# Kernel optimization log

Measured on AMD Instinct MI355X. Metric: run time of the kernel, lower is better.

## Reference

```python
import jax, jax.numpy as jnp
import numpy as np

D_MODEL = 1024
D_FF = 4096


def _layernorm(x, g, b, eps=1e-5):
    mu = jnp.mean(x, axis=-1, keepdims=True)
    var = jnp.var(x, axis=-1, keepdims=True)
    return (x - mu) * jax.lax.rsqrt(var + eps) * g + b


def setup_inputs() -> dict:
    key = jax.random.key(0)
    ks = jax.random.split(key, 16)
    d, f = D_MODEL, D_FF
    s = 1.0 / np.sqrt(d)
    inp = {
        'x': jax.random.normal(ks[0], (4, 2048, d), dtype=jnp.float32),
        'wq': jax.random.uniform(ks[1], (d, d), jnp.float32, -s, s),
        'bq': jax.random.uniform(ks[2], (d,), jnp.float32, -s, s),
        'wk': jax.random.uniform(ks[3], (d, d), jnp.float32, -s, s),
        'bk': jax.random.uniform(ks[4], (d,), jnp.float32, -s, s),
        'wv': jax.random.uniform(ks[5], (d, d), jnp.float32, -s, s),
        'bv': jax.random.uniform(ks[6], (d,), jnp.float32, -s, s),
        'wo': jax.random.uniform(ks[7], (d, d), jnp.float32, -s, s),
        'bo': jax.random.uniform(ks[8], (d,), jnp.float32, -s, s),
        'w1': jax.random.uniform(ks[9], (d, f), jnp.float32, -s, s),
        'b1': jax.random.uniform(ks[10], (f,), jnp.float32, -s, s),
        'w2': jax.random.uniform(ks[11], (f, d), jnp.float32, -1.0 / np.sqrt(f), 1.0 / np.sqrt(f)),
        'b2': jax.random.uniform(ks[12], (d,), jnp.float32, -1.0 / np.sqrt(f), 1.0 / np.sqrt(f)),
        'g1': jnp.ones((d,), jnp.float32),
        'be1': jnp.zeros((d,), jnp.float32),
        'g2': jnp.ones((d,), jnp.float32),
        'be2': jnp.zeros((d,), jnp.float32),
    }
    return inp


def reference(x, wq, bq, wk, bk, wv, bv, wo, bo, w1, b1, w2, b2, g1, be1, g2, be2):
    d_k = x.shape[-1]
    q = jnp.einsum('bsd,de->bse', x, wq) + bq
    k = jnp.einsum('bsd,de->bse', x, wk) + bk
    v = jnp.einsum('bsd,de->bse', x, wv) + bv
    # full-width attention (no head split in the original module)
    scores = jnp.einsum('bqd,bkd->bqk', q, k) / jnp.sqrt(jnp.float32(d_k))
    attn = jax.nn.softmax(scores, axis=-1)
    ctx = jnp.einsum('bqk,bkd->bqd', attn, v)
    attn_out = jnp.einsum('bsd,de->bse', ctx, wo) + bo
    x1 = _layernorm(x + attn_out, g1, be1)
    ff = jnp.einsum('bsf,fd->bsd', jax.nn.relu(jnp.einsum('bsd,df->bsf', x1, w1) + b1), w2) + b2
    return _layernorm(x1 + ff, g2, be2)
```

## Files before the change

kernel.cpp:

```cpp
#include <hip/hip_runtime.h>
#include <stdint.h>


using f32x4 = __attribute__((ext_vector_type(4))) float;
using s16x8 = __attribute__((ext_vector_type(8))) short;

__device__ __forceinline__ ushort f2b(float f) {
    union { float f; uint32_t u; } v; v.f = f;
    uint32_t u = v.u;
    return (ushort)((u + 0x7fffu + ((u >> 16) & 1u)) >> 16);
}
__device__ __forceinline__ float b2f(ushort b) {
    union { uint32_t u; float f; } v; v.u = ((uint32_t)b) << 16;
    return v.f;
}
__device__ __forceinline__ float to_f(float f) { return f; }
__device__ __forceinline__ float to_f(ushort b) { return b2f(b); }

__device__ __forceinline__ void async_ld16(const ushort* g, ushort* l) {
    __builtin_amdgcn_global_load_lds(
        (const __attribute__((address_space(1))) void*)g,
        (__attribute__((address_space(3))) void*)l,
        16, 0, 0);
}

#define WAITCNT_VM4    0x0F74
#define WAITCNT_VM0    0x0F70
#define WAITCNT_LGKM0  0xC07F


__global__ __launch_bounds__(256) void cast_f2b4(const float* __restrict__ src,
                                                 ushort* __restrict__ dst,
                                                 long long n4) {
    long long i = (long long)blockIdx.x * 256 + threadIdx.x;
    if (i >= n4) return;
    float4 f = ((const float4*)src)[i];
    ushort4 o;
    o.x = f2b(f.x); o.y = f2b(f.y); o.z = f2b(f.z); o.w = f2b(f.w);
    ((ushort4*)dst)[i] = o;
}


__global__ __launch_bounds__(256) void concat3(const float* __restrict__ a,
                                               const float* __restrict__ b,
                                               const float* __restrict__ c,
                                               float* __restrict__ dst) {
    int i = blockIdx.x * 256 + threadIdx.x;
    const float* s = (i < 1024) ? a : (i < 2048) ? b : c;
    dst[i] = s[i & 1023];
}


__global__ __launch_bounds__(256) void add2_cast(const float* __restrict__ a,
                                                 const float* __restrict__ b,
                                                 ushort* __restrict__ o,
                                                 long long n4) {
    long long i = (long long)blockIdx.x * 256 + threadIdx.x;
    if (i >= n4) return;
    float4 x = ((const float4*)a)[i];
    float4 y = ((const float4*)b)[i];
    ushort4 u;
    u.x = f2b(x.x + y.x); u.y = f2b(x.y + y.y);
    u.z = f2b(x.z + y.z); u.w = f2b(x.w + y.w);
    ((ushort4*)o)[i] = u;
}


template <typename T>
__global__ __launch_bounds__(256) void transpose_to_bf16(const T* __restrict__ src,
                                                         ushort* __restrict__ dst,
                                                         int R, int C, int srcLd,
                                                         long long ss, long long ds) {
    __shared__ float tile[32][33];
    src += (long long)blockIdx.z * ss;
    dst += (long long)blockIdx.z * ds;
    const int c0 = blockIdx.x * 32;
    const int r0 = blockIdx.y * 32;
    const int tx = threadIdx.x, ty = threadIdx.y;
#pragma unroll
    for (int i = 0; i < 4; i++) {
        int r = r0 + ty + i * 8;
        tile[ty + i * 8][tx] = to_f(src[(long long)r * srcLd + c0 + tx]);
    }
    __syncthreads();
#pragma unroll
    for (int i = 0; i < 4; i++) {
        int r = c0 + ty + i * 8;
        dst[(long long)r * R + r0 + tx] = f2b(tile[tx][ty + i * 8]);
    }
}


__global__ __launch_bounds__(256) void transpose4_to_bf16(const float* __restrict__ s0,
                                                          const float* __restrict__ s1,
                                                          const float* __restrict__ s2,
                                                          const float* __restrict__ s3,
                                                          ushort* __restrict__ dst) {
    __shared__ float tile[32][33];
    const int D = 1024;
    const int z = blockIdx.z;
    const float* src = (z == 0) ? s0 : (z == 1) ? s1 : (z == 2) ? s2 : s3;
    dst += (long long)z * D * D;
    const int c0 = blockIdx.x * 32;
    const int r0 = blockIdx.y * 32;
    const int tx = threadIdx.x, ty = threadIdx.y;
#pragma unroll
    for (int i = 0; i < 4; i++) {
        int r = r0 + ty + i * 8;
        tile[ty + i * 8][tx] = src[(long long)r * D + c0 + tx];
    }
    __syncthreads();
#pragma unroll
    for (int i = 0; i < 4; i++) {
        int r = c0 + ty + i * 8;
        dst[(long long)r * D + r0 + tx] = f2b(tile[tx][ty + i * 8]);
    }
}


template <int OUT_BF16, int RELU, int HAS_BIAS>
__global__ __launch_bounds__(512, 2) void gemm256(const ushort* __restrict__ A,
                                                  const ushort* __restrict__ BT,
                                                  void* __restrict__ Cp,
                                                  const float* __restrict__ bias,
                                                  int K, int kChunks, float scale,
                                                  int lda, int ldb, int ldc,
                                                  long long sA, long long sB,
                                                  long long sC, long long sK) {
    __shared__ ushort SH[65536];
    ushort* Asl = SH;
    ushort* Bsl = SH + 32768;

    const int tid = threadIdx.x;
    const int kIdx = blockIdx.z % kChunks;
    const int bz = blockIdx.z / kChunks;
    const int kLen = K / kChunks;
    const int kOff = kIdx * kLen;
    const int kTiles = kLen >> 5;
    const ushort* Ab = A + (long long)bz * sA;
    const ushort* Bb = BT + (long long)bz * sB;

    const int W = gridDim.x, H = gridDim.y;
    const int bidx = blockIdx.y * W + blockIdx.x;
    const int Hp = H >> 3;
    const int xcd = bidx & 7;
    const int sb = bidx >> 3;
    const int tn = sb / Hp;
    const int tm = xcd * Hp + sb % Hp;

    const int lane = tid & 63;
    const int w = tid >> 6;
    const int wm = w >> 2;
    const int wn = w & 3;
    const int l16 = lane & 15;
    const int quad = lane >> 4;

    const int lr = lane >> 2;
    const int lc = ((lane & 3) ^ ((lane >> 3) & 3)) * 8;
    const ushort* AgS = Ab + (long long)(tm * 256 + w * 32 + lr) * lda + kOff + lc;
    const ushort* BgS = Bb + (long long)(tn * 256 + w * 32 + lr) * ldb + kOff + lc;
    ushort* AsW = Asl + w * 1024;
    ushort* BsW = Bsl + w * 1024;
    const long long rstepA = (long long)16 * lda;
    const long long rstepB = (long long)16 * ldb;

#define STG_AU(tt, boff) { const ushort* ga_ = AgS + (tt) * 32;                   \
        async_ld16(ga_, AsW + (boff));                                            \
        async_ld16(ga_ + rstepA, AsW + (boff) + 512); }
#define STG_BU(tt, boff) { const ushort* gb_ = BgS + (tt) * 32;                   \
        async_ld16(gb_, BsW + (boff));                                            \
        async_ld16(gb_ + rstepB, BsW + (boff) + 512); }

    const int fsl = (quad ^ ((l16 >> 1) & 3)) * 8;
    const ushort* ArdB = Asl + (wm * 128 + l16) * 32 + fsl;
    const ushort* BrdB = Bsl + (wn * 64 + l16) * 32 + fsl;

#define LDA4(dst, boff, ib) {                                                     \
    _Pragma("unroll") for (int i_ = 0; i_ < 4; i_++)                              \
        dst[i_] = *(const s16x8*)(ArdB + (boff) + ((ib) + i_) * 512); }
#define LDB4(dst, boff) {                                                         \
    _Pragma("unroll") for (int j_ = 0; j_ < 4; j_++)                              \
        dst[j_] = *(const s16x8*)(BrdB + (boff) + j_ * 512); }
#define MM16(asrc, bsrc, io) {                                                    \
    _Pragma("unroll") for (int i_ = 0; i_ < 4; i_++)                              \
    _Pragma("unroll") for (int j_ = 0; j_ < 4; j_++)                              \
        acc[(io) + i_][j_] = __builtin_amdgcn_mfma_f32_16x16x32_bf16(             \
            asrc[i_], bsrc[j_], acc[(io) + i_][j_], 0, 0, 0); }

#define BAR   __builtin_amdgcn_s_barrier()
#define PRIO1 __builtin_amdgcn_s_setprio(1)
#define PRIO0 __builtin_amdgcn_s_setprio(0)
#define WVM4  __builtin_amdgcn_s_waitcnt(WAITCNT_VM4)
#define WVM0  __builtin_amdgcn_s_waitcnt(WAITCNT_VM0)
#define WLG0  __builtin_amdgcn_s_waitcnt(WAITCNT_LGKM0)

#define PAIR(c0, c1, d0, d1, t2, t3, LAST) {                                      \
                              \
    LDA4(fa, c0, 0); LDB4(fb0, c0);                                               \
    if (!(LAST)) STG_AU(t2, d0);                                                  \
    BAR; WLG0; PRIO1; MM16(fa, fb0, 0); PRIO0; BAR;                               \
     \
    LDA4(fa2, c0, 4);                                                             \
    if (!(LAST)) STG_BU(t2, d0);                                                  \
    BAR; WLG0; PRIO1; MM16(fa2, fb0, 4); PRIO0;                                   \
    if (LAST) { WVM0; } else { WVM4; }                                            \
    BAR;                                                                          \
                              \
    LDA4(fa, c1, 0); LDB4(fb1, c1);                                               \
    if (!(LAST)) STG_AU(t3, d1);                                                  \
    BAR; WLG0; PRIO1; MM16(fa, fb1, 0); PRIO0; BAR;                               \
     \
    LDA4(fa2, c1, 4);                                                             \
    if (!(LAST)) STG_BU(t3, d1);                                                  \
    BAR; WLG0; PRIO1; MM16(fa2, fb1, 4); PRIO0;                                   \
    if (!(LAST)) { WVM4; }                                                        \
    BAR; }

    f32x4 acc[8][4];
#pragma unroll
    for (int i = 0; i < 8; i++)
#pragma unroll
        for (int j = 0; j < 4; j++) acc[i][j] = (f32x4){0.f, 0.f, 0.f, 0.f};

    s16x8 fa[4], fa2[4], fb0[4], fb1[4];

    STG_AU(0, 0); STG_BU(0, 0); STG_AU(1, 8192); STG_BU(1, 8192);
    WVM4;
    BAR;

    const int nP = kTiles >> 1;
    int pr = 0;
    for (; pr + 3 <= nP; pr += 2) {
        PAIR(0, 8192, 16384, 24576, 2 * pr + 2, 2 * pr + 3, 0);
        PAIR(16384, 24576, 0, 8192, 2 * pr + 4, 2 * pr + 5, 0);
    }
    PAIR(0, 8192, 16384, 24576, 2 * pr + 2, 2 * pr + 3, 0);
    PAIR(16384, 24576, 0, 8192, 0, 0, 1);

#undef STG_AU
#undef STG_BU
#undef LDA4
#undef LDB4
#undef MM16
#undef PAIR

    BAR;

    const long long cb = (long long)bz * sC + (long long)kIdx * sK;
    if (OUT_BF16) {
        ushort* Cb = (ushort*)Cp;
#pragma unroll
        for (int j = 0; j < 4; j++) {
            const int cg = wn * 4 + j;
            const float bv = HAS_BIAS ? bias[tn * 256 + cg * 16 + l16] : 0.0f;
#pragma unroll
            for (int i = 0; i < 8; i++) {
                const int rbase = wm * 128 + i * 16 + quad * 4;
#pragma unroll
                for (int r = 0; r < 4; r++) {
                    const int row = rbase + r;
                    float v = acc[i][j][r] * scale + bv;
                    if (RELU) v = v > 0.f ? v : 0.f;
                    SH[row * 256 + ((cg ^ ((row >> 2) & 3)) << 4) + l16] = f2b(v);
                }
            }
        }
        BAR;
        const int crow = tid >> 5;
        const int cch = tid & 31;
        const int g = cch >> 1, hh = cch & 1;
#pragma unroll
        for (int pass = 0; pass < 16; pass++) {
            const int row = pass * 16 + crow;
            s16x8 vv = *(const s16x8*)&SH[row * 256 + ((g ^ ((row >> 2) & 3)) << 4) + hh * 8];
            *(s16x8*)&Cb[cb + (long long)(tm * 256 + row) * ldc + tn * 256 + cch * 8] = vv;
        }
    } else {
        float* Cf = (float*)Cp;
        float* SHf = (float*)SH;
#pragma unroll
        for (int half = 0; half < 2; half++) {
            if (wm == half) {
#pragma unroll
                for (int j = 0; j < 4; j++) {
                    const int col = wn * 64 + j * 16 + l16;
                    const float bv = (HAS_BIAS && kIdx == 0) ? bias[tn * 256 + col] : 0.0f;
                    const int gg = col >> 3, cl = col & 7;
#pragma unroll
                    for (int i = 0; i < 8; i++) {
                        const int rbase = i * 16 + quad * 4;
#pragma unroll
                        for (int r = 0; r < 4; r++) {
                            const int row = rbase + r;
                            float v = acc[i][j][r] * scale + bv;
                            if (RELU) v = v > 0.f ? v : 0.f;
                            SHf[row * 256 + ((gg ^ ((row >> 2) & 3)) << 3) + cl] = v;
                        }
                    }
                }
            }
            BAR;
            const int rr = tid >> 6, cc = tid & 63;
            const int g2 = cc >> 1, h2 = cc & 1;
#pragma unroll
            for (int pass = 0; pass < 16; pass++) {
                const int row = pass * 8 + rr;
                f32x4 vv = *(const f32x4*)&SHf[row * 256 + ((g2 ^ ((row >> 2) & 3)) << 3) + h2 * 4];
                *(f32x4*)&Cf[cb + (long long)(tm * 256 + half * 128 + row) * ldc + tn * 256 + cc * 4] = vv;
            }
            BAR;
        }
    }
#undef BAR
#undef PRIO1
#undef PRIO0
#undef WVM4
#undef WVM0
#undef WLG0
}


__global__ __launch_bounds__(256) void softmax_rows(const ushort* __restrict__ S,
                                                    ushort* __restrict__ P) {
    const int C = 2048;
    const long long row = blockIdx.x;
    const int tid = threadIdx.x;
    const ushort4* s4 = (const ushort4*)(S + row * C) + tid * 2;
    ushort4 a = s4[0], bq = s4[1];
    float v[8];
    v[0] = b2f(a.x); v[1] = b2f(a.y); v[2] = b2f(a.z); v[3] = b2f(a.w);
    v[4] = b2f(bq.x); v[5] = b2f(bq.y); v[6] = b2f(bq.z); v[7] = b2f(bq.w);
    float mx = -1e30f;
#pragma unroll
    for (int i = 0; i < 8; i++) mx = fmaxf(mx, v[i]);
    __shared__ float red[256];
    red[tid] = mx;
    __syncthreads();
    for (int off = 128; off > 0; off >>= 1) {
        if (tid < off) red[tid] = fmaxf(red[tid], red[tid + off]);
        __syncthreads();
    }
    mx = red[0];
    __syncthreads();
    float sum = 0.f;
#pragma unroll
    for (int i = 0; i < 8; i++) {
        v[i] = __expf(v[i] - mx);
        sum += v[i];
    }
    red[tid] = sum;
    __syncthreads();
    for (int off = 128; off > 0; off >>= 1) {
        if (tid < off) red[tid] += red[tid + off];
        __syncthreads();
    }
    float inv = 1.f / red[0];
    ushort4 o0, o1;
    o0.x = f2b(v[0] * inv); o0.y = f2b(v[1] * inv); o0.z = f2b(v[2] * inv); o0.w = f2b(v[3] * inv);
    o1.x = f2b(v[4] * inv); o1.y = f2b(v[5] * inv); o1.z = f2b(v[6] * inv); o1.w = f2b(v[7] * inv);
    ushort4* p4 = (ushort4*)(P + row * C) + tid * 2;
    p4[0] = o0;
    p4[1] = o1;
}


__global__ __launch_bounds__(256) void residual_ln(const float* __restrict__ X,
                                                   const float* __restrict__ Y,
                                                   const float* __restrict__ Y2,
                                                   const float* __restrict__ g,
                                                   const float* __restrict__ be,
                                                   float* __restrict__ outf,
                                                   ushort* __restrict__ outb) {
    const int D = 1024;
    const long long row = blockIdx.x;
    const float* x = X + row * D;
    const float* y = Y + row * D;
    const float* y2 = Y2 ? Y2 + row * D : nullptr;
    const int tid = threadIdx.x;
    float v[4];
    float s = 0.f, s2 = 0.f;
#pragma unroll
    for (int i = 0; i < 4; i++) {
        int c = tid + i * 256;
        float t = x[c] + y[c];
        if (y2) t += y2[c];
        v[i] = t;
        s += t;
        s2 += t * t;
    }
    __shared__ float r1[256], r2[256];
    r1[tid] = s;
    r2[tid] = s2;
    __syncthreads();
    for (int off = 128; off > 0; off >>= 1) {
        if (tid < off) {
            r1[tid] += r1[tid + off];
            r2[tid] += r2[tid + off];
        }
        __syncthreads();
    }
    float mu = r1[0] * (1.f / 1024.f);
    float var = r2[0] * (1.f / 1024.f) - mu * mu;
    float inv = rsqrtf(var + 1e-5f);
    float* of = outf + row * D;
    ushort* ob = outb ? outb + row * D : nullptr;
#pragma unroll
    for (int i = 0; i < 4; i++) {
        int c = tid + i * 256;
        float o = (v[i] - mu) * inv * g[c] + be[c];
        of[c] = o;
        if (ob) ob[c] = f2b(o);
    }
}


extern "C" void kernel_launch(void* const* d_in, const int* in_sizes, int n_in,
                              void* d_out, int out_size, void* d_ws, size_t ws_size,
                              hipStream_t stream) {
    const float* x  = (const float*)d_in[0];
    const float* wq = (const float*)d_in[1];
    const float* bq = (const float*)d_in[2];
    const float* wk = (const float*)d_in[3];
    const float* bk = (const float*)d_in[4];
    const float* wv = (const float*)d_in[5];
    const float* bv = (const float*)d_in[6];
    const float* wo = (const float*)d_in[7];
    const float* bo = (const float*)d_in[8];
    const float* w1 = (const float*)d_in[9];
    const float* b1 = (const float*)d_in[10];
    const float* w2 = (const float*)d_in[11];
    const float* b2 = (const float*)d_in[12];
    const float* g1 = (const float*)d_in[13];
    const float* be1 = (const float*)d_in[14];
    const float* g2 = (const float*)d_in[15];
    const float* be2 = (const float*)d_in[16];
    float* out = (float*)d_out;
    char* ws = (char*)d_ws;

    const int Bz = 4, S = 2048, D = 1024, F = 4096;
    const int T = Bz * S;
    const size_t MBy = 1024ull * 1024ull;

    ushort* qkvT = (ushort*)(ws + 0);
    ushort* woT  = (ushort*)(ws + 6 * MBy);
    ushort* w1T  = (ushort*)(ws + 8 * MBy);
    ushort* w2T  = (ushort*)(ws + 16 * MBy);
    float*  bqkv = (float*)(ws + 24 * MBy);
    ushort* xb   = (ushort*)(ws + 25 * MBy);
    ushort* qkv  = (ushort*)(ws + 41 * MBy);
    ushort* vT   = (ushort*)(ws + 89 * MBy);
    ushort* scb  = (ushort*)(ws + 105 * MBy);
    ushort* attn = (ushort*)(ws + 169 * MBy);
    float*  ctx0 = (float*)(ws + 105 * MBy);
    float*  ctx1 = (float*)(ws + 137 * MBy);
    ushort* ctxb = (ushort*)(ws + 25 * MBy);
    float*  ao0 = (float*)(ws + 105 * MBy);
    float*  ao1 = (float*)(ws + 137 * MBy);
    float*  x1  = (float*)(ws + 41 * MBy);
    ushort* x1b = (ushort*)(ws + 73 * MBy);
    ushort* h   = (ushort*)(ws + 105 * MBy);
    float*  ff0 = (float*)(ws + 169 * MBy);
    float*  ff1 = (float*)(ws + 73 * MBy);

    dim3 b32(32, 8);

    cast_f2b4<<<(T * D) / 1024, 256, 0, stream>>>(x, xb, (long long)(T * D) / 4);

    transpose4_to_bf16<<<dim3(32, 32, 4), b32, 0, stream>>>(wq, wk, wv, wo, qkvT);
    transpose_to_bf16<float><<<dim3(128, 32, 1), b32, 0, stream>>>(w1, w1T, D, F, F, 0, 0);
    transpose_to_bf16<float><<<dim3(32, 128, 1), b32, 0, stream>>>(w2, w2T, F, D, D, 0, 0);

    concat3<<<12, 256, 0, stream>>>(bq, bk, bv, bqkv);

    gemm256<1, 0, 1><<<dim3(3 * D / 256, T / 256, 1), 512, 0, stream>>>(
        xb, qkvT, qkv, bqkv, D, 1, 1.f, D, D, 3 * D, 0, 0, 0, 0);

    transpose_to_bf16<ushort><<<dim3(D / 32, S / 32, Bz), b32, 0, stream>>>(
        qkv + 2048, vT, S, D, 3 * D, (long long)S * 3 * D, (long long)S * D);

    gemm256<1, 0, 0><<<dim3(S / 256, S / 256, Bz), 512, 0, stream>>>(
        qkv, qkv + 1024, scb, nullptr, D, 1, 0.03125f, 3 * D, 3 * D, S,
        (long long)S * 3 * D, (long long)S * 3 * D, (long long)S * S, 0);

    softmax_rows<<<T, 256, 0, stream>>>(scb, attn);

    gemm256<0, 0, 0><<<dim3(D / 256, S / 256, Bz * 2), 512, 0, stream>>>(
        attn, vT, ctx0, nullptr, S, 2, 1.f, S, S, D,
        (long long)S * S, (long long)D * S, (long long)S * D, (long long)(ctx1 - ctx0));

    add2_cast<<<(T * D) / 1024, 256, 0, stream>>>(ctx0, ctx1, ctxb, (long long)(T * D) / 4);

    gemm256<0, 0, 1><<<dim3(D / 256, T / 256, 2), 512, 0, stream>>>(
        ctxb, woT, ao0, bo, D, 2, 1.f, D, D, D, 0, 0, 0, (long long)(ao1 - ao0));

    residual_ln<<<T, 256, 0, stream>>>(x, ao0, ao1, g1, be1, x1, x1b);

    gemm256<1, 1, 1><<<dim3(F / 256, T / 256, 1), 512, 0, stream>>>(
        x1b, w1T, h, b1, D, 1, 1.f, D, D, F, 0, 0, 0, 0);

    gemm256<0, 0, 1><<<dim3(D / 256, T / 256, 2), 512, 0, stream>>>(
        h, w2T, ff0, b2, F, 2, 1.f, F, F, D, 0, 0, 0, (long long)(ff1 - ff0));

    residual_ln<<<T, 256, 0, stream>>>(x1, ff0, ff1, g2, be2, out, nullptr);
}
```

Measured before the change: 539.1 us.

## Switch GEMM inner loop to 32x32x16 MFMA and vectorize residual layernorm

Replaces the 16x16x32 bf16 MFMA tiling (8x4 accumulators per wave) with 32x32x16 MFMA (4x2 f32x16 accumulators), changing the LDS fragment addressing, the K-split within each 32-wide tile and the epilogue row/column mapping. This cuts the number of LDS fragment loads and MFMA issues per tile, which should lower LDS traffic and instruction overhead. Separately, the residual layernorm kernel now uses float4 loads and stores instead of strided scalar accesses. The risk is an error in the new lane-to-element mapping, and the 32x32 instruction's different latency may interact with the existing barrier and priority schedule.

After: 579.4 us. +7.5%, slower.

```diff
diff --git a/kernel.cpp b/kernel.cpp
--- a/kernel.cpp
+++ b/kernel.cpp
@@ -3,6 +3,7 @@
 
 
 using f32x4 = __attribute__((ext_vector_type(4))) float;
+using f32x16 = __attribute__((ext_vector_type(16))) float;
 using s16x8 = __attribute__((ext_vector_type(8))) short;
 
 __device__ __forceinline__ ushort f2b(float f) {
@@ -152,8 +153,8 @@
     const int w = tid >> 6;
     const int wm = w >> 2;
     const int wn = w & 3;
-    const int l16 = lane & 15;
-    const int quad = lane >> 4;
+    const int lcol = lane & 31;
+    const int lhi = lane >> 5;
 
     const int lr = lane >> 2;
     const int lc = ((lane & 3) ^ ((lane >> 3) & 3)) * 8;
@@ -171,21 +172,23 @@
         async_ld16(gb_, BsW + (boff));                                            \
         async_ld16(gb_ + rstepB, BsW + (boff) + 512); }
 
-    const int fsl = (quad ^ ((l16 >> 1) & 3)) * 8;
-    const ushort* ArdB = Asl + (wm * 128 + l16) * 32 + fsl;
-    const ushort* BrdB = Bsl + (wn * 64 + l16) * 32 + fsl;
-
-#define LDA4(dst, boff, ib) {                                                     \
+    const int fsl0 = ((lhi) ^ ((lcol >> 1) & 3)) * 8;
+    const ushort* ArdB0 = Asl + (wm * 128 + lcol) * 32 + fsl0;
+    const ushort* ArdB1 = Asl + (wm * 128 + lcol) * 32 + (fsl0 ^ 16);
+    const ushort* BrdB0 = Bsl + (wn * 64 + lcol) * 32 + fsl0;
+    const ushort* BrdB1 = Bsl + (wn * 64 + lcol) * 32 + (fsl0 ^ 16);
+
+#define LDA4(base, boff) {                                                        \
     _Pragma("unroll") for (int i_ = 0; i_ < 4; i_++)                              \
-        dst[i_] = *(const s16x8*)(ArdB + (boff) + ((ib) + i_) * 512); }
-#define LDB4(dst, boff) {                                                         \
-    _Pragma("unroll") for (int j_ = 0; j_ < 4; j_++)                              \
-        dst[j_] = *(const s16x8*)(BrdB + (boff) + j_ * 512); }
-#define MM16(asrc, bsrc, io) {                                                    \
-    _Pragma("unroll") for (int i_ = 0; i_ < 4; i_++)                              \
-    _Pragma("unroll") for (int j_ = 0; j_ < 4; j_++)                              \
-        acc[(io) + i_][j_] = __builtin_amdgcn_mfma_f32_16x16x32_bf16(             \
-            asrc[i_], bsrc[j_], acc[(io) + i_][j_], 0, 0, 0); }
+        fa[i_] = *(const s16x8*)(base + (boff) + i_ * 1024); }
+#define LDB2(base, boff) {                                                        \
+    _Pragma("unroll") for (int j_ = 0; j_ < 2; j_++)                              \
+        fb[j_] = *(const s16x8*)(base + (boff) + j_ * 1024); }
+#define MM8() {                                                                   \
+    _Pragma("unroll") for (int tm_ = 0; tm_ < 4; tm_++)                           \
+    _Pragma("unroll") for (int tn_ = 0; tn_ < 2; tn_++)                           \
+        acc[tm_][tn_] = __builtin_amdgcn_mfma_f32_32x32x16_bf16(                  \
+            fa[tm_], fb[tn_], acc[tm_][tn_], 0, 0, 0); }
 
 #define BAR   __builtin_amdgcn_s_barrier()
 #define PRIO1 __builtin_amdgcn_s_setprio(1)
@@ -195,34 +198,34 @@
 #define WLG0  __builtin_amdgcn_s_waitcnt(WAITCNT_LGKM0)
 
 #define PAIR(c0, c1, d0, d1, t2, t3, LAST) {                                      \
-                              \
-    LDA4(fa, c0, 0); LDB4(fb0, c0);                                               \
+                                          \
+    LDA4(ArdB0, c0); LDB2(BrdB0, c0);                                             \
     if (!(LAST)) STG_AU(t2, d0);                                                  \
-    BAR; WLG0; PRIO1; MM16(fa, fb0, 0); PRIO0; BAR;                               \
-     \
-    LDA4(fa2, c0, 4);                                                             \
+    BAR; WLG0; PRIO1; MM8(); PRIO0; BAR;                                          \
+            \
+    LDA4(ArdB1, c0); LDB2(BrdB1, c0);                                             \
     if (!(LAST)) STG_BU(t2, d0);                                                  \
-    BAR; WLG0; PRIO1; MM16(fa2, fb0, 4); PRIO0;                                   \
+    BAR; WLG0; PRIO1; MM8(); PRIO0;                                               \
     if (LAST) { WVM0; } else { WVM4; }                                            \
     BAR;                                                                          \
-                              \
-    LDA4(fa, c1, 0); LDB4(fb1, c1);                                               \
+                                          \
+    LDA4(ArdB0, c1); LDB2(BrdB0, c1);                                             \
     if (!(LAST)) STG_AU(t3, d1);                                                  \
-    BAR; WLG0; PRIO1; MM16(fa, fb1, 0); PRIO0; BAR;                               \
-     \
-    LDA4(fa2, c1, 4);                                                             \
+    BAR; WLG0; PRIO1; MM8(); PRIO0; BAR;                                          \
+            \
+    LDA4(ArdB1, c1); LDB2(BrdB1, c1);                                             \
     if (!(LAST)) STG_BU(t3, d1);                                                  \
-    BAR; WLG0; PRIO1; MM16(fa2, fb1, 4); PRIO0;                                   \
+    BAR; WLG0; PRIO1; MM8(); PRIO0;                                               \
     if (!(LAST)) { WVM4; }                                                        \
     BAR; }
 
-    f32x4 acc[8][4];
-#pragma unroll
-    for (int i = 0; i < 8; i++)
-#pragma unroll
-        for (int j = 0; j < 4; j++) acc[i][j] = (f32x4){0.f, 0.f, 0.f, 0.f};
-
-    s16x8 fa[4], fa2[4], fb0[4], fb1[4];
+    f32x16 acc[4][2];
+#pragma unroll
+    for (int i = 0; i < 4; i++)
+#pragma unroll
+        for (int j = 0; j < 2; j++) acc[i][j] = (f32x16){0.f};
+
+    s16x8 fa[4], fb[2];
 
     STG_AU(0, 0); STG_BU(0, 0); STG_AU(1, 8192); STG_BU(1, 8192);
     WVM4;
@@ -240,8 +243,8 @@
 #undef STG_AU
 #undef STG_BU
 #undef LDA4
-#undef LDB4
-#undef MM16
+#undef LDB2
+#undef MM8
 #undef PAIR
 
     BAR;
@@ -250,18 +253,19 @@
     if (OUT_BF16) {
         ushort* Cb = (ushort*)Cp;
 #pragma unroll
-        for (int j = 0; j < 4; j++) {
-            const int cg = wn * 4 + j;
-            const float bv = HAS_BIAS ? bias[tn * 256 + cg * 16 + l16] : 0.0f;
-#pragma unroll
-            for (int i = 0; i < 8; i++) {
-                const int rbase = wm * 128 + i * 16 + quad * 4;
-#pragma unroll
-                for (int r = 0; r < 4; r++) {
-                    const int row = rbase + r;
-                    float v = acc[i][j][r] * scale + bv;
+        for (int tn_ = 0; tn_ < 2; tn_++) {
+            const int col = wn * 64 + tn_ * 32 + lcol;
+            const float bv = HAS_BIAS ? bias[tn * 256 + col] : 0.0f;
+            const int cg = col >> 4, cl16 = col & 15;
+#pragma unroll
+            for (int tm_ = 0; tm_ < 4; tm_++) {
+                const int rbase = wm * 128 + tm_ * 32 + 4 * lhi;
+#pragma unroll
+                for (int r = 0; r < 16; r++) {
+                    const int row = rbase + (r & 3) + 8 * (r >> 2);
+                    float v = acc[tm_][tn_][r] * scale + bv;
                     if (RELU) v = v > 0.f ? v : 0.f;
-                    SH[row * 256 + ((cg ^ ((row >> 2) & 3)) << 4) + l16] = f2b(v);
+                    SH[row * 256 + ((cg ^ ((row >> 2) & 3)) << 4) + cl16] = f2b(v);
                 }
             }
         }
@@ -282,17 +286,17 @@
         for (int half = 0; half < 2; half++) {
             if (wm == half) {
 #pragma unroll
-                for (int j = 0; j < 4; j++) {
-                    const int col = wn * 64 + j * 16 + l16;
+                for (int tn_ = 0; tn_ < 2; tn_++) {
+                    const int col = wn * 64 + tn_ * 32 + lcol;
                     const float bv = (HAS_BIAS && kIdx == 0) ? bias[tn * 256 + col] : 0.0f;
                     const int gg = col >> 3, cl = col & 7;
 #pragma unroll
-                    for (int i = 0; i < 8; i++) {
-                        const int rbase = i * 16 + quad * 4;
-#pragma unroll
-                        for (int r = 0; r < 4; r++) {
-                            const int row = rbase + r;
-                            float v = acc[i][j][r] * scale + bv;
+                    for (int tm_ = 0; tm_ < 4; tm_++) {
+                        const int rbase = tm_ * 32 + 4 * lhi;
+#pragma unroll
+                        for (int r = 0; r < 16; r++) {
+                            const int row = rbase + (r & 3) + 8 * (r >> 2);
+                            float v = acc[tm_][tn_][r] * scale + bv;
                             if (RELU) v = v > 0.f ? v : 0.f;
                             SHf[row * 256 + ((gg ^ ((row >> 2) & 3)) << 3) + cl] = v;
                         }
@@ -373,21 +377,16 @@
                                                    ushort* __restrict__ outb) {
     const int D = 1024;
     const long long row = blockIdx.x;
-    const float* x = X + row * D;
-    const float* y = Y + row * D;
-    const float* y2 = Y2 ? Y2 + row * D : nullptr;
     const int tid = threadIdx.x;
-    float v[4];
-    float s = 0.f, s2 = 0.f;
-#pragma unroll
-    for (int i = 0; i < 4; i++) {
-        int c = tid + i * 256;
-        float t = x[c] + y[c];
-        if (y2) t += y2[c];
-        v[i] = t;
-        s += t;
-        s2 += t * t;
-    }
+    float4 xv = ((const float4*)(X + row * D))[tid];
+    float4 yv = ((const float4*)(Y + row * D))[tid];
+    xv.x += yv.x; xv.y += yv.y; xv.z += yv.z; xv.w += yv.w;
+    if (Y2) {
+        float4 y2v = ((const float4*)(Y2 + row * D))[tid];
+        xv.x += y2v.x; xv.y += y2v.y; xv.z += y2v.z; xv.w += y2v.w;
+    }
+    float s = xv.x + xv.y + xv.z + xv.w;
+    float s2 = xv.x * xv.x + xv.y * xv.y + xv.z * xv.z + xv.w * xv.w;
     __shared__ float r1[256], r2[256];
     r1[tid] = s;
     r2[tid] = s2;
@@ -402,14 +401,18 @@
     float mu = r1[0] * (1.f / 1024.f);
     float var = r2[0] * (1.f / 1024.f) - mu * mu;
     float inv = rsqrtf(var + 1e-5f);
-    float* of = outf + row * D;
-    ushort* ob = outb ? outb + row * D : nullptr;
-#pragma unroll
-    for (int i = 0; i < 4; i++) {
-        int c = tid + i * 256;
-        float o = (v[i] - mu) * inv * g[c] + be[c];
-        of[c] = o;
-        if (ob) ob[c] = f2b(o);
+    float4 gv = ((const float4*)g)[tid];
+    float4 bv = ((const float4*)be)[tid];
+    float4 o;
+    o.x = (xv.x - mu) * inv * gv.x + bv.x;
+    o.y = (xv.y - mu) * inv * gv.y + bv.y;
+    o.z = (xv.z - mu) * inv * gv.z + bv.z;
+    o.w = (xv.w - mu) * inv * gv.w + bv.w;
+    ((float4*)(outf + row * D))[tid] = o;
+    if (outb) {
+        ushort4 u;
+        u.x = f2b(o.x); u.y = f2b(o.y); u.z = f2b(o.z); u.w = f2b(o.w);
+        ((ushort4*)(outb + row * D))[tid] = u;
     }
 }
 
```
